# Kernel tuning notes

Hardware: AMD Instinct MI355X
Metric: run time of the kernel (lower is better)

The kernel has to match this reference:

```python
import jax, jax.numpy as jnp
import numpy as np

N_SERIES = 100000
INPUT_SIZE = 28
OUTPUT_SIZE = 7
N_T = 1
N_S = 4
PERIOD = 7            # seasonality = [7]
EMBED = 1 + 1 + PERIOD  # lev_sms, seas_sms, init seasonal factors
BATCH = 2048
N_TIME = 2048


def setup_inputs() -> dict:
    key = jax.random.key(0)
    k1, k2, k3, k4 = jax.random.split(key, 4)
    # Y must be strictly positive (multiplicative model: division + log)
    Y = jax.random.uniform(k1, (BATCH, N_TIME), dtype=jnp.float32, minval=0.5, maxval=1.5)
    X = jax.random.normal(k2, (BATCH, N_T, N_TIME), dtype=jnp.float32)
    S = jax.random.normal(k3, (BATCH, N_S), dtype=jnp.float32)
    idxs = jax.random.randint(k4, (BATCH,), 0, N_SERIES)
    embeds_weight = jnp.full((N_SERIES, EMBED), 0.5, dtype=jnp.float32)
    return {"S": S, "Y": Y, "X": X, "idxs": idxs,
            "embeds_weight": embeds_weight, "step_size": 7}


def _levels_seasons(Y, idxs, embeds_weight):
    """Exponential smoothing level/seasonality recurrence (single seasonality)."""
    emb = embeds_weight[idxs]                      # (B, 9)
    lev_sms = jax.nn.sigmoid(emb[:, 0])            # (B,)
    seas_sms = jax.nn.sigmoid(emb[:, 1])           # (B,)
    init_seas = jnp.exp(emb[:, 2:2 + PERIOD])      # (B, 7)

    level0 = Y[:, 0] / init_seas[:, 0]
    # ring buffer holding the seasonal factors used at steps t=1..: [s1..s6, s0]
    buf0 = jnp.concatenate([init_seas[:, 1:], init_seas[:, :1]], axis=1)  # (B, 7)

    def step(carry, inp):
        lev, buf = carry
        y, k = inp
        s = jnp.take(buf, k % PERIOD, axis=1)                       # seasonality at lag PERIOD
        newlev = lev_sms * (y / s) + (1.0 - lev_sms) * lev
        news = seas_sms * (y / newlev) + (1.0 - seas_sms) * s
        buf = jax.lax.dynamic_update_slice_in_dim(buf, news[:, None], k % PERIOD, axis=1)
        return (newlev, buf), (newlev, news)

    ks = jnp.arange(N_TIME - 1, dtype=jnp.int32)
    (_, _), (levs, seas) = jax.lax.scan(step, (level0, buf0), (Y[:, 1:].T, ks))
    levels = jnp.concatenate([level0[:, None], levs.T], axis=1)           # (B, n_time)
    seasonal = jnp.concatenate([init_seas, init_seas[:, :1], seas.T], axis=1)  # (B, n_time+7)
    return levels, seasonal


def reference(S, Y, X, idxs, embeds_weight, step_size):
    levels, seasonal = _levels_seasons(Y, idxs, embeds_weight)

    windows_end = N_TIME - INPUT_SIZE - OUTPUT_SIZE + 1
    windows = np.arange(0, windows_end, step_size)          # static window starts
    W = len(windows)

    # --- insample windows, normalized: log(Y / level / season) ---
    idx_in = windows[:, None] + np.arange(INPUT_SIZE)       # (W, I)
    Yw = Y[:, idx_in]                                       # (B, W, I)
    lev_w = levels[:, windows + INPUT_SIZE - 1]             # (B, W)
    seas_w = seasonal[:, idx_in]                            # (B, W, I)
    y_in = jnp.log(Yw / (lev_w[:, :, None] * seas_w))
    y_in = y_in.transpose(1, 0, 2)                          # (W, B, I)

    # --- exogenous windows: X[:, :, start:start+I+O].reshape(B, -1) ---
    idx_x = windows[:, None] + np.arange(INPUT_SIZE + OUTPUT_SIZE)  # (W, I+O)
    Xw = X[:, :, idx_x].transpose(2, 0, 1, 3).reshape(W, BATCH, N_T * (INPUT_SIZE + OUTPUT_SIZE))

    # --- static features ---
    Sw = jnp.broadcast_to(S[None], (W, BATCH, N_S))

    windows_y_insample = jnp.concatenate([y_in, Xw, Sw], axis=2)   # (W, B, context)

    # --- outsample windows (eval mode: not normalized) ---
    idx_out = windows[:, None] + INPUT_SIZE + np.arange(OUTPUT_SIZE)  # (W, O)
    windows_y_outsample = Y[:, idx_out].transpose(1, 0, 2)            # (W, B, O)

    return windows_y_insample, windows_y_outsample, levels, seasonal
```

## Files before the change

### kernel.cpp

```cpp
#include <hip/hip_runtime.h>
#include <math.h>

#define BATCH 2048
#define N_TIME 2048
#define INPUT_SIZE 28
#define OUTPUT_SIZE 7
#define N_S 4
#define PERIOD 7
#define EMBED 9
#define SEAS_LEN (N_TIME + PERIOD)
#define W_COUNT 288
#define WB_COUNT (W_COUNT * BATCH)
#define INS_COLS 67
#define OUT0_SIZE (WB_COUNT * INS_COLS)
#define OUT1_SIZE (WB_COUNT * OUTPUT_SIZE)
#define LEV_SIZE (BATCH * N_TIME)
#define SEAS_SIZE (BATCH * SEAS_LEN)

struct ScanState {
    float lev, lsms, seas_sms, oma, oms;
    float sbuf[PERIOD];
    float rbuf[PERIOD];
    float yp, sp, rnlp, rnsp;
};

template<bool FIRST, bool LAST, bool PREF>
__device__ __forceinline__ void scan_chunk(
    int base, int l, int r0, int jr, int km,
    const float* __restrict__ Yb,
    float (&cur)[64], float (&nxt)[64],
    float (*__restrict__ tl)[65], float (*__restrict__ ts)[65],
    ScanState& st,
    float* __restrict__ levels, float* __restrict__ seasonal)
{
    if (PREF) {
#pragma unroll
        for (int k = 0; k < 64; k += 4)
            *(float4*)&nxt[k] = *(const float4*)(Yb + base + 64 + k);
    }
    tl[l][0] = st.lev;
#pragma unroll
    for (int k = 0; k < 64; ++k) {
        if (!LAST || k < 63) {
            float y  = (k < 63) ? cur[k + 1] : nxt[0];
            float s0 = st.sbuf[0];
            float nl = fmaf(st.oma, st.lev, y * st.rbuf[0]);
            st.lev = nl;
            tl[l][k + 1] = nl;
            if (!FIRST || k > 0) {
                float u  = st.yp * st.rnlp;
                float ns = fmaf(st.oms, st.sp, st.seas_sms * u);
                ts[l][k] = ns;
                st.sbuf[PERIOD - 1] = ns;
                if (!FIRST || k > 1)
                    st.rbuf[PERIOD - 2] = st.lsms * st.rnsp;
                st.rnsp = __builtin_amdgcn_rcpf(ns);
            }
            float rnl = __builtin_amdgcn_rcpf(nl);
#pragma unroll
            for (int q = 0; q < PERIOD - 1; ++q) st.sbuf[q] = st.sbuf[q + 1];
#pragma unroll
            for (int q = 0; q < PERIOD - 1; ++q) st.rbuf[q] = st.rbuf[q + 1];
            st.yp = y; st.sp = s0; st.rnlp = rnl;
        }
    }
    if (LAST) {
        float u  = st.yp * st.rnlp;
        float ns = fmaf(st.oms, st.sp, st.seas_sms * u);
        ts[l][63] = ns;
    }
    asm volatile("s_waitcnt lgkmcnt(0)" ::: "memory");
#pragma unroll
    for (int j0 = 0; j0 < 64; j0 += 4) {
        int j = j0 + jr;
        float vl[4], vs[4];
#pragma unroll
        for (int i = 0; i < 4; ++i) { vl[i] = tl[j][km + i]; vs[i] = ts[j][km + i]; }
        float4 v4; v4.x = vl[0]; v4.y = vl[1]; v4.z = vl[2]; v4.w = vl[3];
        *(float4*)(levels + (size_t)(r0 + j) * N_TIME + base + km) = v4;
        float* srow = seasonal + (size_t)(r0 + j) * SEAS_LEN + base + 7 + km;
#pragma unroll
        for (int i = 0; i < 4; ++i) srow[i] = vs[i];
    }
    asm volatile("s_waitcnt lgkmcnt(0)" ::: "memory");
}

__global__ __launch_bounds__(64) void es_scan(
    const float* __restrict__ Y, const int* __restrict__ idxs,
    const float* __restrict__ emb,
    float* __restrict__ levels, float* __restrict__ seasonal)
{
    __shared__ float tl[64][65];
    __shared__ float ts[64][65];
    const int l  = threadIdx.x;
    const int r0 = blockIdx.x * 64;
    const int b  = r0 + l;
    const float* Yb = Y + (size_t)b * N_TIME;
    const int jr = l >> 4;
    const int km = (l & 15) * 4;

    const float* e = emb + (size_t)idxs[b] * EMBED;
    ScanState st;
    st.lsms     = 1.0f / (1.0f + __expf(-e[0]));
    st.seas_sms = 1.0f / (1.0f + __expf(-e[1]));
    st.oma = 1.0f - st.lsms;
    st.oms = 1.0f - st.seas_sms;
    float is[PERIOD];
#pragma unroll
    for (int j = 0; j < PERIOD; ++j) is[j] = __expf(e[2 + j]);
    st.lev = Yb[0] / is[0];

    float* seab = seasonal + (size_t)b * SEAS_LEN;
#pragma unroll
    for (int j = 0; j < PERIOD; ++j) seab[j] = is[j];
    ts[l][0] = is[0];
#pragma unroll
    for (int j = 0; j < PERIOD; ++j) st.sbuf[j] = is[(j + 1) % PERIOD];
#pragma unroll
    for (int j = 0; j < PERIOD; ++j)
        st.rbuf[j] = st.lsms * __builtin_amdgcn_rcpf(st.sbuf[j]);
    st.yp = 0.0f; st.sp = 1.0f; st.rnlp = 1.0f; st.rnsp = 1.0f;

    float ya[64], yb2[64];
#pragma unroll
    for (int k = 0; k < 64; k += 4)
        *(float4*)&ya[k] = *(const float4*)(Yb + k);

    scan_chunk<true,  false, true >(0, l, r0, jr, km, Yb, ya, yb2, tl, ts, st, levels, seasonal);
#pragma unroll 1
    for (int cc = 0; cc < 15; ++cc) {
        scan_chunk<false, false, true>(64  + cc * 128, l, r0, jr, km, Yb, yb2, ya, tl, ts, st, levels, seasonal);
        scan_chunk<false, false, true>(128 + cc * 128, l, r0, jr, km, Yb, ya, yb2, tl, ts, st, levels, seasonal);
    }
    scan_chunk<false, true,  false>(1984, l, r0, jr, km, Yb, yb2, ya, tl, ts, st, levels, seasonal);
}

__global__ __launch_bounds__(256) void es_windows(
    const float* __restrict__ Y, const float* __restrict__ X,
    const float* __restrict__ S, const float* __restrict__ levels,
    const float* __restrict__ seasonal,
    float* __restrict__ out0, float* __restrict__ out1)
{
    int gid = blockIdx.x * 256 + threadIdx.x;
    if (gid < OUT0_SIZE) {
        unsigned u  = (unsigned)gid;
        unsigned wb = u / 67u;
        int j  = (int)(u - wb * 67u);
        int w  = (int)(wb >> 11);
        int b  = (int)(wb & (BATCH - 1));
        int t0 = w * 7;
        float v;
        if (j < INPUT_SIZE) {
            float y  = Y[b * N_TIME + t0 + j];
            float lv = levels[b * N_TIME + t0 + INPUT_SIZE - 1];
            float sv = seasonal[b * SEAS_LEN + t0 + j];
            v = __logf(y * __builtin_amdgcn_rcpf(lv * sv));
        } else if (j < 63) {
            v = X[b * N_TIME + t0 + (j - INPUT_SIZE)];
        } else {
            v = S[b * N_S + (j - 63)];
        }
        out0[gid] = v;
    } else {
        unsigned e  = (unsigned)(gid - OUT0_SIZE);
        unsigned wb = e / 7u;
        int m  = (int)(e - wb * 7u);
        int w  = (int)(wb >> 11);
        int b  = (int)(wb & (BATCH - 1));
        out1[e] = Y[b * N_TIME + w * 7 + INPUT_SIZE + m];
    }
}

extern "C" void kernel_launch(void* const* d_in, const int* in_sizes, int n_in,
                              void* d_out, int out_size, void* d_ws, size_t ws_size,
                              hipStream_t stream) {
    const float* S    = (const float*)d_in[0];
    const float* Y    = (const float*)d_in[1];
    const float* X    = (const float*)d_in[2];
    const int*   idxs = (const int*)d_in[3];
    const float* emb  = (const float*)d_in[4];

    float* out      = (float*)d_out;
    float* out_ins  = out;
    float* out_outs = out + OUT0_SIZE;
    float* levels   = out + OUT0_SIZE + OUT1_SIZE;
    float* seasonal = out + OUT0_SIZE + OUT1_SIZE + LEV_SIZE;

    es_scan<<<BATCH / 64, 64, 0, stream>>>(Y, idxs, emb, levels, seasonal);

    const int total = OUT0_SIZE + OUT1_SIZE;
    es_windows<<<total / 256, 256, 0, stream>>>(
        Y, X, S, levels, seasonal, out_ins, out_outs);
}
```

Measured before the change: 414.6 us.

## Split scan kernel into producer and drain waves with double-buffered LDS

The es_scan block grows to two wavefronts. One wave runs the serial level/seasonal recurrence and writes each 64-step chunk into one of two LDS buffers. The second wave transposes the previous chunk out of LDS and writes it to global memory, and a barrier per chunk keeps the two waves in lockstep. This takes the global store and transpose work off the latency-bound recurrence path, at the cost of a block-wide barrier per chunk and twice the LDS.

```diff
diff --git a/kernel.cpp b/kernel.cpp
--- a/kernel.cpp
+++ b/kernel.cpp
@@ -26,12 +26,11 @@
 
 template<bool FIRST, bool LAST, bool PREF>
 __device__ __forceinline__ void scan_chunk(
-    int base, int l, int r0, int jr, int km,
+    int base, int l,
     const float* __restrict__ Yb,
     float (&cur)[64], float (&nxt)[64],
     float (*__restrict__ tl)[65], float (*__restrict__ ts)[65],
-    ScanState& st,
-    float* __restrict__ levels, float* __restrict__ seasonal)
+    ScanState& st)
 {
     if (PREF) {
 #pragma unroll
@@ -70,6 +69,16 @@
         ts[l][63] = ns;
     }
     asm volatile("s_waitcnt lgkmcnt(0)" ::: "memory");
+    __builtin_amdgcn_s_barrier();
+}
+
+__device__ __forceinline__ void drain_chunk(
+    int base, int jr, int km, int r0,
+    const float (*__restrict__ tl)[65], const float (*__restrict__ ts)[65],
+    float* __restrict__ levels, float* __restrict__ seasonal)
+{
+    __builtin_amdgcn_s_barrier();
+    asm volatile("" ::: "memory");
 #pragma unroll
     for (int j0 = 0; j0 < 64; j0 += 4) {
         int j = j0 + jr;
@@ -85,54 +94,61 @@
     asm volatile("s_waitcnt lgkmcnt(0)" ::: "memory");
 }
 
-__global__ __launch_bounds__(64) void es_scan(
+__global__ __launch_bounds__(128) void es_scan(
     const float* __restrict__ Y, const int* __restrict__ idxs,
     const float* __restrict__ emb,
     float* __restrict__ levels, float* __restrict__ seasonal)
 {
-    __shared__ float tl[64][65];
-    __shared__ float ts[64][65];
-    const int l  = threadIdx.x;
-    const int r0 = blockIdx.x * 64;
-    const int b  = r0 + l;
-    const float* Yb = Y + (size_t)b * N_TIME;
-    const int jr = l >> 4;
-    const int km = (l & 15) * 4;
-
-    const float* e = emb + (size_t)idxs[b] * EMBED;
-    ScanState st;
-    st.lsms     = 1.0f / (1.0f + __expf(-e[0]));
-    st.seas_sms = 1.0f / (1.0f + __expf(-e[1]));
-    st.oma = 1.0f - st.lsms;
-    st.oms = 1.0f - st.seas_sms;
-    float is[PERIOD];
-#pragma unroll
-    for (int j = 0; j < PERIOD; ++j) is[j] = __expf(e[2 + j]);
-    st.lev = Yb[0] / is[0];
-
-    float* seab = seasonal + (size_t)b * SEAS_LEN;
-#pragma unroll
-    for (int j = 0; j < PERIOD; ++j) seab[j] = is[j];
-    ts[l][0] = is[0];
-#pragma unroll
-    for (int j = 0; j < PERIOD; ++j) st.sbuf[j] = is[(j + 1) % PERIOD];
-#pragma unroll
-    for (int j = 0; j < PERIOD; ++j)
-        st.rbuf[j] = st.lsms * __builtin_amdgcn_rcpf(st.sbuf[j]);
-    st.yp = 0.0f; st.sp = 1.0f; st.rnlp = 1.0f; st.rnsp = 1.0f;
-
-    float ya[64], yb2[64];
-#pragma unroll
-    for (int k = 0; k < 64; k += 4)
-        *(float4*)&ya[k] = *(const float4*)(Yb + k);
-
-    scan_chunk<true,  false, true >(0, l, r0, jr, km, Yb, ya, yb2, tl, ts, st, levels, seasonal);
+    __shared__ float tl[2][64][65];
+    __shared__ float ts[2][64][65];
+    const int tid = threadIdx.x;
+    const int l   = tid & 63;
+    const int r0  = blockIdx.x * 64;
+
+    if (tid < 64) {
+        const int b = r0 + l;
+        const float* Yb = Y + (size_t)b * N_TIME;
+        const float* e  = emb + (size_t)idxs[b] * EMBED;
+        ScanState st;
+        st.lsms     = 1.0f / (1.0f + __expf(-e[0]));
+        st.seas_sms = 1.0f / (1.0f + __expf(-e[1]));
+        st.oma = 1.0f - st.lsms;
+        st.oms = 1.0f - st.seas_sms;
+        float is[PERIOD];
+#pragma unroll
+        for (int j = 0; j < PERIOD; ++j) is[j] = __expf(e[2 + j]);
+        st.lev = Yb[0] / is[0];
+
+        float* seab = seasonal + (size_t)b * SEAS_LEN;
+#pragma unroll
+        for (int j = 0; j < PERIOD; ++j) seab[j] = is[j];
+        ts[0][l][0] = is[0];
+#pragma unroll
+        for (int j = 0; j < PERIOD; ++j) st.sbuf[j] = is[(j + 1) % PERIOD];
+#pragma unroll
+        for (int j = 0; j < PERIOD; ++j)
+            st.rbuf[j] = st.lsms * __builtin_amdgcn_rcpf(st.sbuf[j]);
+        st.yp = 0.0f; st.sp = 1.0f; st.rnlp = 1.0f; st.rnsp = 1.0f;
+
+        float ya[64], yb2[64];
+#pragma unroll
+        for (int k = 0; k < 64; k += 4)
+            *(float4*)&ya[k] = *(const float4*)(Yb + k);
+
+        scan_chunk<true,  false, true >(0, l, Yb, ya, yb2, tl[0], ts[0], st);
 #pragma unroll 1
-    for (int cc = 0; cc < 15; ++cc) {
-        scan_chunk<false, false, true>(64  + cc * 128, l, r0, jr, km, Yb, yb2, ya, tl, ts, st, levels, seasonal);
-        scan_chunk<false, false, true>(128 + cc * 128, l, r0, jr, km, Yb, ya, yb2, tl, ts, st, levels, seasonal);
-    }
-    scan_chunk<false, true,  false>(1984, l, r0, jr, km, Yb, yb2, ya, tl, ts, st, levels, seasonal);
+        for (int cc = 0; cc < 15; ++cc) {
+            scan_chunk<false, false, true>(64  + cc * 128, l, Yb, yb2, ya, tl[1], ts[1], st);
+            scan_chunk<false, false, true>(128 + cc * 128, l, Yb, ya, yb2, tl[0], ts[0], st);
+        }
+        scan_chunk<false, true,  false>(1984, l, Yb, yb2, ya, tl[1], ts[1], st);
+    } else {
+        const int jr = l >> 4;
+        const int km = (l & 15) * 4;
+#pragma unroll 1
+        for (int c = 0; c < 32; ++c)
+            drain_chunk(c * 64, jr, km, r0, tl[c & 1], ts[c & 1], levels, seasonal);
+    }
 }
 
 __global__ __launch_bounds__(256) void es_windows(
@@ -186,7 +202,7 @@
     float* levels   = out + OUT0_SIZE + OUT1_SIZE;
     float* seasonal = out + OUT0_SIZE + OUT1_SIZE + LEV_SIZE;
 
-    es_scan<<<BATCH / 64, 64, 0, stream>>>(Y, idxs, emb, levels, seasonal);
+    es_scan<<<BATCH / 64, 128, 0, stream>>>(Y, idxs, emb, levels, seasonal);
 
     const int total = OUT0_SIZE + OUT1_SIZE;
     es_windows<<<total / 256, 256, 0, stream>>>(
```

After: 356.5 us. -14.0%, faster.
